# Performance work log

Measured on AMD Instinct MI355X. Metric: run time of the kernel, lower is better.

Reference implementation:

```python
import jax, jax.numpy as jnp
import numpy as np

BN_EPS = 1e-5


def _tconv(X, w1, b1, w2, b2, w3, b3):
    # X: (B, T, N, C) -> conv over time with kernel (1, k), gated GLU-style
    Xp = X.transpose(0, 2, 1, 3)  # (B, N, T, C)
    def conv(w, b):
        return jax.lax.conv_general_dilated(
            Xp, w, (1, 1), 'VALID',
            dimension_numbers=('NHWC', 'HWIO', 'NHWC')) + b
    P = conv(w1, b1)
    Q = jax.nn.sigmoid(conv(w2, b2))
    R = conv(w3, b3)
    H = jax.nn.relu(P * Q + R)
    return H.transpose(0, 2, 1, 3)  # (B, T-k+1, N, Cout)


def _cheb(x, ei, W, b):
    # Batched ChebConv (sym norm, lambda_max=2 => L_hat = -D^-1/2 A D^-1/2)
    # x: (S, N, F), ei: (S, 2, E), W: (K, F, Fout)
    S, N, F = x.shape
    row, col = ei[:, 0], ei[:, 1]           # (S, E)
    ones = jnp.ones(ei.shape[-1], x.dtype)
    def norm_one(r, c):
        deg = jax.ops.segment_sum(ones, r, num_segments=N)
        dis = jnp.where(deg > 0, jax.lax.rsqrt(jnp.maximum(deg, 1.)), 0.)
        return -dis[r] * dis[c]
    w = jax.vmap(norm_one)(row, col)        # (S, E), constant wrt floats
    def prop(xs, r, c, ws):
        return jax.ops.segment_sum(ws[:, None] * xs[c], r, num_segments=N)
    propv = jax.vmap(prop)
    Tx = [x, propv(x, row, col, w)]
    for _ in range(W.shape[0] - 2):
        Tx.append(2. * propv(Tx[-1], row, col, w) - Tx[-2])
    return jnp.einsum('ksnf,kfo->sno', jnp.stack(Tx), W) + b


def _forward(X, tc1_w1, tc1_b1, tc1_w2, tc1_b2, tc1_w3, tc1_b3,
             cheb_w, cheb_b,
             tc2_w1, tc2_b1, tc2_w2, tc2_b2, tc2_w3, tc2_b3,
             bn_gamma, bn_beta, conv3_w, conv3_b, f1_w, f1_b, edge_index):
    T0 = _tconv(X, tc1_w1, tc1_b1, tc1_w2, tc1_b2, tc1_w3, tc1_b3)  # (B,38,N,H)
    B, Tt, N, H = T0.shape
    ei = edge_index[:, :Tt].reshape(B * Tt, 2, edge_index.shape[-1])
    G = _cheb(T0.reshape(B * Tt, N, H), ei, cheb_w, cheb_b)
    G = jax.nn.relu(G.reshape(B, Tt, N, H))
    T2 = _tconv(G, tc2_w1, tc2_b1, tc2_w2, tc2_b2, tc2_w3, tc2_b3)  # (B,36,N,Co)
    # BatchNorm2d over channel dim = num_nodes (training-mode batch stats)
    Tn = T2.transpose(0, 2, 1, 3)  # (B, N, T, C)
    mean = Tn.mean(axis=(0, 2, 3), keepdims=True)
    var = Tn.var(axis=(0, 2, 3), keepdims=True)
    Tn = (Tn - mean) * jax.lax.rsqrt(var + BN_EPS)
    Tn = Tn * bn_gamma[None, :, None, None] + bn_beta[None, :, None, None]
    Tb = Tn.transpose(0, 2, 1, 3)                 # (B, T, N, C)
    Tr = Tb.reshape(B, Tb.shape[1], -1)           # (B, T, N*C=3200)
    y = jax.lax.conv_general_dilated(
        Tr[:, None, :, :], conv3_w, (1, 1), 'VALID',
        dimension_numbers=('NCHW', 'OIHW', 'NCHW'))  # (B,128,T-2,1)
    y = y + conv3_b[None, :, None, None]
    y = y[:, :, :, 0]
    pooled = y.mean(axis=2)                        # AvgPool1d over full length
    return pooled @ f1_w + f1_b                    # (B, 3200)


def setup_inputs() -> dict:
    key = jax.random.key(0)
    ks = jax.random.split(key, 20)
    B, Tw, N, Cin, H, Co, E = 32, 40, 50, 2, 128, 64, 800
    KT, K = 3, 3
    s = 0.05
    d = {
        'X': jax.random.normal(ks[0], (B, Tw, N, Cin), jnp.float32),
        'edge_index': jax.random.randint(ks[1], (B, Tw, 2, E), 0, N),
        'tc1_w1': jax.random.normal(ks[2], (1, KT, Cin, H), jnp.float32) * s,
        'tc1_b1': jnp.zeros((H,), jnp.float32),
        'tc1_w2': jax.random.normal(ks[3], (1, KT, Cin, H), jnp.float32) * s,
        'tc1_b2': jnp.zeros((H,), jnp.float32),
        'tc1_w3': jax.random.normal(ks[4], (1, KT, Cin, H), jnp.float32) * s,
        'tc1_b3': jnp.zeros((H,), jnp.float32),
        'cheb_w': jax.random.normal(ks[5], (K, H, H), jnp.float32) * s,
        'cheb_b': jnp.zeros((H,), jnp.float32),
        'tc2_w1': jax.random.normal(ks[6], (1, KT, H, Co), jnp.float32) * s,
        'tc2_b1': jnp.zeros((Co,), jnp.float32),
        'tc2_w2': jax.random.normal(ks[7], (1, KT, H, Co), jnp.float32) * s,
        'tc2_b2': jnp.zeros((Co,), jnp.float32),
        'tc2_w3': jax.random.normal(ks[8], (1, KT, H, Co), jnp.float32) * s,
        'tc2_b3': jnp.zeros((Co,), jnp.float32),
        'bn_gamma': jnp.ones((N,), jnp.float32),
        'bn_beta': jnp.zeros((N,), jnp.float32),
        'conv3_w': jax.random.normal(ks[9], (128, 1, 3, N * Co), jnp.float32) * 0.01,
        'conv3_b': jnp.zeros((128,), jnp.float32),
        'f1_w': jax.random.normal(ks[10], (128, N * Co), jnp.float32) * s,
        'f1_b': jnp.zeros((N * Co,), jnp.float32),
    }
    return d


def reference(X, tc1_w1, tc1_b1, tc1_w2, tc1_b2, tc1_w3, tc1_b3,
              cheb_w, cheb_b,
              tc2_w1, tc2_b1, tc2_w2, tc2_b2, tc2_w3, tc2_b3,
              bn_gamma, bn_beta, conv3_w, conv3_b, f1_w, f1_b, edge_index):
    return _forward(X, tc1_w1, tc1_b1, tc1_w2, tc1_b2, tc1_w3, tc1_b3,
                    cheb_w, cheb_b,
                    tc2_w1, tc2_b1, tc2_w2, tc2_b2, tc2_w3, tc2_b3,
                    bn_gamma, bn_beta, conv3_w, conv3_b, f1_w, f1_b, edge_index)
```

## Files before the change

### kernel.cpp

```cpp
#include <hip/hip_runtime.h>
#include <hip/hip_bf16.h>

#define BB 32
#define TW 40
#define NN 50
#define HH 128
#define CO 64
#define EE 800
#define TT 38
#define TT2 36
#define TPOOL 34
#define NCO 3200
#define SS (BB*TT)
#define NPAD 64
#define RPAD (SS*NPAD)

#define PB_US ((size_t)RPAD * HH)
#define PB_BYTES (PB_US * 2)

typedef __attribute__((ext_vector_type(8))) short s16x8;
typedef __attribute__((ext_vector_type(16))) float f32x16;
typedef unsigned short us;

static __device__ __forceinline__ unsigned int f2bf_u(float x) {
    unsigned int u = __float_as_uint(x);
    return (u + 0x7fffu + ((u >> 16) & 1u)) >> 16;
}
static __device__ __forceinline__ float bfu2f(unsigned int h) {
    return __uint_as_float(h << 16);
}
static __device__ __forceinline__ size_t fragoff32(int m, int c) {
    return (size_t)(c >> 4) * 512 + ((c >> 3) & 1) * 256 + m * 8 + (c & 7);
}
#define MFMA(a, b, c) __builtin_amdgcn_mfma_f32_32x32x16_bf16((a), (b), (c), 0, 0, 0)

__global__ __launch_bounds__(256) void k_wprep(
    const float* __restrict__ cw,
    const float* __restrict__ tw1, const float* __restrict__ tw2, const float* __restrict__ tw3,
    us* __restrict__ VTh, us* __restrict__ VTl,
    us* __restrict__ WTh,
    float* __restrict__ pooled)
{
    int idx = blockIdx.x * 256 + threadIdx.x;
    float v; int col, k; bool wantlo;
    us *dh, *dl;
    if (idx < 128 * 384) {
        col = idx / 384; k = idx % 384;
        if (k < 128)      v = cw[k * 128 + col] - cw[32768 + k * 128 + col];
        else if (k < 256) v = cw[16384 + (k - 128) * 128 + col];
        else              v = 2.f * cw[32768 + (k - 256) * 128 + col];
        dh = VTh; dl = VTl; wantlo = true;
    } else if (idx < 128 * 384 + 192 * 384) {
        int i2 = idx - 128 * 384;
        col = i2 / 384; k = i2 % 384;
        int gg = col >> 6, o = col & 63;
        const float* src = (gg == 0) ? tw1 : (gg == 1) ? tw2 : tw3;
        v = src[k * 64 + o];
        dh = WTh; dl = 0; wantlo = false;
    } else {
        int z = idx - (128 * 384 + 192 * 384);
        if (z < 4096) pooled[z] = 0.f;
        return;
    }
    size_t off = ((size_t)((col >> 5) * 24 + (k >> 4)) * 64 + ((k >> 3) & 1) * 32 + (col & 31)) * 8
               + (k & 7);
    unsigned int h = f2bf_u(v);
    dh[off] = (us)h;
    if (wantlo) dl[off] = (us)f2bf_u(v - bfu2f(h));
}

#define TAS 136
#define TBS 72
#define LMS 53
__global__ __launch_bounds__(256) void k_cheb(
    const int* __restrict__ EI, const float* __restrict__ X,
    const float* __restrict__ w1, const float* __restrict__ b1,
    const float* __restrict__ w2, const float* __restrict__ b2,
    const float* __restrict__ w3, const float* __restrict__ b3,
    const us* __restrict__ VTh, const us* __restrict__ VTl,
    const float* __restrict__ bias,
    us* __restrict__ Gh)
{
    __shared__ __align__(16) char smem[61440];
    us* TbA = (us*)smem;
    us* TbB = (us*)(smem + 17408);
    us* Pa  = (us*)(smem + 35840);
    float* Lm = (float*)(smem + 35840);
    us* LA  = (us*)(smem + 53248);
    float* Xs = (float*)(smem + 53248);
    int* deg  = (int*)(smem + 53248 + 1216);
    float* dis = (float*)(smem + 53248 + 1216 + 224);

    int g = blockIdx.x;
    int tid = threadIdx.x;
    int b = g / TT, t = g % TT;
    const int* row = EI + (size_t)(b * TW + t) * 2 * EE;
    const int* col = row + EE;

    {
        s16x8 zz = {0, 0, 0, 0, 0, 0, 0, 0};
        for (int i = tid; i < 2240; i += 256) ((s16x8*)smem)[i] = zz;
    }
    for (int i = tid; i < 52 * LMS; i += 256) Lm[i] = 0.f;
    for (int i = tid; i < 300; i += 256) Xs[i] = X[(size_t)(b * TW + t) * 100 + i];
    if (tid < NN) deg[tid] = 0;
    __syncthreads();

    {
        int c = tid & 127, nh = tid >> 7;
        float wr1[6], wr2[6], wr3[6];
#pragma unroll
        for (int q = 0; q < 6; q++) {
            wr1[q] = w1[q * HH + c];
            wr2[q] = w2[q * HH + c];
            wr3[q] = w3[q * HH + c];
        }
        float bv1 = b1[c], bv2 = b2[c], bv3 = b3[c];
        for (int n = nh; n < NN; n += 2) {
            float P = bv1, Q = bv2, R = bv3;
#pragma unroll
            for (int q = 0; q < 6; q++) {
                float x = Xs[(q >> 1) * 100 + n * 2 + (q & 1)];
                P += x * wr1[q]; Q += x * wr2[q]; R += x * wr3[q];
            }
            float sg = 1.f / (1.f + expf(-Q));
            float v = P * sg + R;
            v = v > 0.f ? v : 0.f;
            us h = (us)f2bf_u(v);
            TbA[n * TAS + c] = h;
            TbB[c * TBS + n] = h;
        }
    }
    __syncthreads();
    for (int e = tid; e < EE; e += 256) atomicAdd(&deg[row[e]], 1);
    __syncthreads();
    if (tid < NN) dis[tid] = deg[tid] > 0 ? rsqrtf((float)deg[tid]) : 0.f;
    __syncthreads();
    for (int e = tid; e < EE; e += 256) {
        int r = row[e], cc = col[e];
        atomicAdd(&Lm[r * LMS + cc], -dis[r] * dis[cc]);
    }
    __syncthreads();
    for (int ent = tid; ent < 512; ent += 256) {
        int lanee = ent & 63;
        int ks = (ent >> 6) & 3;
        int mt = ent >> 8;
        int m = mt * 32 + (lanee & 31);
        int kb = ks * 16 + (lanee >> 5) * 8;
        s16x8 v;
#pragma unroll
        for (int j = 0; j < 8; j++) {
            int k = kb + j;
            float lv = (m < NN && k < NN) ? Lm[m * LMS + k] : 0.f;
            v[j] = (short)f2bf_u(lv);
        }
        *(s16x8*)(LA + ent * 8) = v;
    }
    __syncthreads();

    int lane = tid & 63;
    int w = tid >> 6;
    int rg = w >> 1, fh = w & 1;
    int nl = lane & 31;
    int khalf = lane >> 5;
    size_t laneoff = (size_t)lane * 8;

    const us* vh0 = VTh + (size_t)(fh * 2) * 12288 + laneoff;
    const us* vh1 = VTh + (size_t)(fh * 2 + 1) * 12288 + laneoff;
    const us* vl0 = VTl + (size_t)(fh * 2) * 12288 + laneoff;
    const us* vl1 = VTl + (size_t)(fh * 2 + 1) * 12288 + laneoff;

    int mrowA = rg * 32 + nl;
    int kbb = khalf * 8;

    f32x16 gacc0, gacc1, d0, d1;
#pragma unroll
    for (int r = 0; r < 16; r++) { gacc0[r] = 0.f; gacc1[r] = 0.f; d0[r] = 0.f; d1[r] = 0.f; }

#pragma unroll
    for (int ks = 0; ks < 4; ks++) {
        s16x8 afr = *(const s16x8*)(LA + ((rg * 4 + ks) * 64 + lane) * 8);
        int kb = ks * 16 + kbb;
        s16x8 bf0 = *(const s16x8*)(TbB + (fh * 64 + nl) * TBS + kb);
        s16x8 bf1 = *(const s16x8*)(TbB + (fh * 64 + 32 + nl) * TBS + kb);
        d0 = MFMA(afr, bf0, d0);
        d1 = MFMA(afr, bf1, d1);
    }
#pragma unroll
    for (int ks = 0; ks < 8; ks++) {
        s16x8 ah = *(const s16x8*)(TbA + mrowA * TAS + ks * 16 + kbb);
        s16x8 bh0 = *(const s16x8*)(vh0 + ks * 512);
        s16x8 bl0 = *(const s16x8*)(vl0 + ks * 512);
        s16x8 bh1 = *(const s16x8*)(vh1 + ks * 512);
        s16x8 bl1 = *(const s16x8*)(vl1 + ks * 512);
        gacc0 = MFMA(ah, bh0, gacc0); gacc0 = MFMA(ah, bl0, gacc0);
        gacc1 = MFMA(ah, bh1, gacc1); gacc1 = MFMA(ah, bl1, gacc1);
    }
    __syncthreads();
#pragma unroll
    for (int r = 0; r < 16; r++) {
        int mrow = (r & 3) + 8 * (r >> 2) + 4 * khalf;
        int node = rg * 32 + mrow;
        int f0 = fh * 64 + nl, f1 = f0 + 32;
        us h0 = (us)f2bf_u(d0[r]);
        us h1 = (us)f2bf_u(d1[r]);
        Pa[node * TAS + f0] = h0;
        Pa[node * TAS + f1] = h1;
        TbB[f0 * TBS + node] = h0;
        TbB[f1 * TBS + node] = h1;
    }
    __syncthreads();

#pragma unroll
    for (int r = 0; r < 16; r++) { d0[r] = 0.f; d1[r] = 0.f; }
#pragma unroll
    for (int ks = 0; ks < 4; ks++) {
        s16x8 afr = *(const s16x8*)(LA + ((rg * 4 + ks) * 64 + lane) * 8);
        int kb = ks * 16 + kbb;
        s16x8 bf0 = *(const s16x8*)(TbB + (fh * 64 + nl) * TBS + kb);
        s16x8 bf1 = *(const s16x8*)(TbB + (fh * 64 + 32 + nl) * TBS + kb);
        d0 = MFMA(afr, bf0, d0);
        d1 = MFMA(afr, bf1, d1);
    }
#pragma unroll
    for (int ks = 0; ks < 8; ks++) {
        s16x8 ah = *(const s16x8*)(Pa + mrowA * TAS + ks * 16 + kbb);
        s16x8 bh0 = *(const s16x8*)(vh0 + (8 + ks) * 512);
        s16x8 bh1 = *(const s16x8*)(vh1 + (8 + ks) * 512);
        gacc0 = MFMA(ah, bh0, gacc0);
        gacc1 = MFMA(ah, bh1, gacc1);
    }
    __syncthreads();
#pragma unroll
    for (int r = 0; r < 16; r++) {
        int mrow = (r & 3) + 8 * (r >> 2) + 4 * khalf;
        int node = rg * 32 + mrow;
        int f0 = fh * 64 + nl, f1 = f0 + 32;
        Pa[node * TAS + f0] = (us)f2bf_u(d0[r]);
        Pa[node * TAS + f1] = (us)f2bf_u(d1[r]);
    }
    __syncthreads();
#pragma unroll
    for (int ks = 0; ks < 8; ks++) {
        s16x8 ah = *(const s16x8*)(Pa + mrowA * TAS + ks * 16 + kbb);
        s16x8 bh0 = *(const s16x8*)(vh0 + (16 + ks) * 512);
        s16x8 bh1 = *(const s16x8*)(vh1 + (16 + ks) * 512);
        gacc0 = MFMA(ah, bh0, gacc0);
        gacc1 = MFMA(ah, bh1, gacc1);
    }

    int c0 = fh * 64 + nl, c1 = c0 + 32;
    float bv0 = bias[c0], bv1 = bias[c1];
    size_t gb = (size_t)g * 8192 + (size_t)rg * 4096;
#pragma unroll
    for (int r = 0; r < 16; r++) {
        int mrow = (r & 3) + 8 * (r >> 2) + 4 * khalf;
        float v0 = gacc0[r] + bv0; v0 = v0 > 0.f ? v0 : 0.f;
        float v1 = gacc1[r] + bv1; v1 = v1 > 0.f ? v1 : 0.f;
        Gh[gb + fragoff32(mrow, c0)] = (us)f2bf_u(v0);
        Gh[gb + fragoff32(mrow, c1)] = (us)f2bf_u(v1);
    }
}

__global__ __launch_bounds__(128) void k_tc2(
    const us* __restrict__ Gh,
    const us* __restrict__ WTh,
    const float* __restrict__ tb1, const float* __restrict__ tb2, const float* __restrict__ tb3,
    us* __restrict__ T2)
{
    int tid = threadIdx.x;
    int lane = tid & 63;
    int w = tid >> 6;
    int nl = lane & 31;
    size_t laneoff = (size_t)lane * 8;
    int i = blockIdx.x;
    int vb = (i & 7) * 288 + (i >> 3);
    int bt36 = vb >> 1, ntile = vb & 1;
    int b = bt36 / TT2, t = bt36 % TT2;

    const us* A[3];
#pragma unroll
    for (int k3 = 0; k3 < 3; k3++)
        A[k3] = Gh + (size_t)(b * TT + t + k3) * 8192 + (size_t)ntile * 4096 + laneoff;
    const us* Bh[3];
#pragma unroll
    for (int g3 = 0; g3 < 3; g3++)
        Bh[g3] = WTh + (size_t)(g3 * 2 + w) * 12288 + laneoff;

    f32x16 aP, aQ, aR;
#pragma unroll
    for (int r = 0; r < 16; r++) { aP[r] = 0.f; aQ[r] = 0.f; aR[r] = 0.f; }

#pragma unroll
    for (int k3 = 0; k3 < 3; k3++) {
#pragma unroll
        for (int ls = 0; ls < 8; ls++) {
            int offB = (k3 * 8 + ls) * 512;
            s16x8 a0 = *(const s16x8*)(A[k3] + ls * 512);
            s16x8 ph = *(const s16x8*)(Bh[0] + offB);
            s16x8 qh = *(const s16x8*)(Bh[1] + offB);
            s16x8 rh = *(const s16x8*)(Bh[2] + offB);
            aP = MFMA(a0, ph, aP);
            aQ = MFMA(a0, qh, aQ);
            aR = MFMA(a0, rh, aR);
        }
    }

    int o = w * 32 + nl;
    float bP = tb1[o], bQ = tb2[o], bR = tb3[o];
    int rbase = (lane >> 5) * 4;
#pragma unroll
    for (int r = 0; r < 16; r++) {
        int m = (r & 3) + 8 * (r >> 2) + rbase;
        int node = ntile * 32 + m;
        if (node < NN) {
            float P = aP[r] + bP, Q = aQ[r] + bQ, R = aR[r] + bR;
            float sg = 1.f / (1.f + expf(-Q));
            float v = P * sg + R;
            v = v > 0.f ? v : 0.f;
            T2[((size_t)bt36 * NN + node) * CO + o] = (us)f2bf_u(v);
        }
    }
}

#define UPST 129
__global__ __launch_bounds__(256) void k_upool(
    const us* __restrict__ T2,
    const float* __restrict__ gamma, const float* __restrict__ beta,
    const float* __restrict__ W3, float* __restrict__ pooled)
{
    __shared__ float Ws[96 * UPST];
    __shared__ __align__(16) float Ul[96 * 36];
    __shared__ float red[512];
    int blk = blockIdx.x;
    int n = blk >> 1, jh = blk & 1;
    int tid = threadIdx.x;

    for (int i = tid; i < 12288; i += 256) {
        int ok = i >> 5, j = i & 31;
        int o = ok / 3, k = ok - 3 * o;
        Ws[(k * 32 + j) * UPST + o] = W3[(size_t)o * 9600 + k * 3200 + n * 64 + jh * 32 + j];
    }

    float s = 0.f, ss = 0.f;
    for (int i = tid; i < 9216; i += 256) {
        int bt = i >> 3, j8 = i & 7;
        s16x8 v = *(const s16x8*)(T2 + (size_t)bt * 3200 + n * 64 + j8 * 8);
#pragma unroll
        for (int j = 0; j < 8; j++) {
            float f = bfu2f((us)v[j]);
            s += f; ss += f * f;
        }
    }
    red[tid] = s; red[256 + tid] = ss;
    __syncthreads();
    for (int off = 128; off > 0; off >>= 1) {
        if (tid < off) { red[tid] += red[tid + off]; red[256 + tid] += red[256 + tid + off]; }
        __syncthreads();
    }
    const float inv = 1.f / (float)(BB * TT2 * CO);
    float mn = red[0] * inv;
    float var = red[256] * inv - mn * mn;
    float sc = rsqrtf(var + 1e-5f) * gamma[n];
    float offv = (float)TPOOL * beta[n] - (float)TPOOL * mn * sc;
    __syncthreads();

    for (int p = tid; p < 1024; p += 256) {
        int j = p & 31, b = p >> 5;
        const us* q = T2 + (size_t)b * 115200 + n * 64 + jh * 32 + j;
        float s0 = 0.f;
        for (int t = 0; t < TPOOL; t++) s0 += bfu2f(q[(size_t)t * 3200]);
        float s1 = s0 - bfu2f(q[0]) + bfu2f(q[(size_t)34 * 3200]);
        float s2 = s1 - bfu2f(q[(size_t)1 * 3200]) + bfu2f(q[(size_t)35 * 3200]);
        Ul[(0 * 32 + j) * 36 + b] = s0 * sc + offv;
        Ul[(1 * 32 + j) * 36 + b] = s1 * sc + offv;
        Ul[(2 * 32 + j) * 36 + b] = s2 * sc + offv;
    }
    __syncthreads();

    int o = tid & 127, bq = tid >> 7;
    float acc[16];
#pragma unroll
    for (int i = 0; i < 16; i++) acc[i] = 0.f;
    for (int kj = 0; kj < 96; kj++) {
        float wv = Ws[kj * UPST + o];
        const float* up = &Ul[kj * 36 + bq * 16];
#pragma unroll
        for (int i4 = 0; i4 < 4; i4++) {
            float4 u = *(const float4*)(up + i4 * 4);
            acc[i4 * 4 + 0] += wv * u.x;
            acc[i4 * 4 + 1] += wv * u.y;
            acc[i4 * 4 + 2] += wv * u.z;
            acc[i4 * 4 + 3] += wv * u.w;
        }
    }
#pragma unroll
    for (int i = 0; i < 16; i++)
        atomicAdd(&pooled[(size_t)(bq * 16 + i) * 128 + o], acc[i]);
}

__global__ __launch_bounds__(256) void k_final(
    const float* __restrict__ pooled, const float* __restrict__ b3c,
    const float* __restrict__ f1w, const float* __restrict__ f1b,
    float* __restrict__ out)
{
    int idx = blockIdx.x * 256 + threadIdx.x;
    if (idx >= BB * NCO) return;
    int q = idx % NCO;
    int b = idx / NCO;
    const float inv = 1.f / (float)TPOOL;
    float acc = f1b[q];
    const float* pp = pooled + b * 128;
#pragma unroll 4
    for (int o = 0; o < 128; o++) acc += (pp[o] * inv + b3c[o]) * f1w[(size_t)o * NCO + q];
    out[idx] = acc;
}

extern "C" void kernel_launch(void* const* d_in, const int* in_sizes, int n_in,
                              void* d_out, int out_size, void* d_ws, size_t ws_size,
                              hipStream_t stream)
{
    const float* X       = (const float*)d_in[0];
    const int*   EI      = (const int*)d_in[1];
    const float* tc1_w1  = (const float*)d_in[2];
    const float* tc1_b1  = (const float*)d_in[3];
    const float* tc1_w2  = (const float*)d_in[4];
    const float* tc1_b2  = (const float*)d_in[5];
    const float* tc1_w3  = (const float*)d_in[6];
    const float* tc1_b3  = (const float*)d_in[7];
    const float* cheb_w  = (const float*)d_in[8];
    const float* cheb_b  = (const float*)d_in[9];
    const float* tc2_w1  = (const float*)d_in[10];
    const float* tc2_b1  = (const float*)d_in[11];
    const float* tc2_w2  = (const float*)d_in[12];
    const float* tc2_b2  = (const float*)d_in[13];
    const float* tc2_w3  = (const float*)d_in[14];
    const float* tc2_b3  = (const float*)d_in[15];
    const float* bn_g    = (const float*)d_in[16];
    const float* bn_b    = (const float*)d_in[17];
    const float* conv3_w = (const float*)d_in[18];
    const float* conv3_b = (const float*)d_in[19];
    const float* f1_w    = (const float*)d_in[20];
    const float* f1_b    = (const float*)d_in[21];

    char* base = (char*)d_ws;
    us*    Gh     = (us*)base;
    us*    T2     = (us*)(base + PB_BYTES);
    float* pooled = (float*)(base + PB_BYTES + 7372800);
    us*    VTh    = (us*)(base + PB_BYTES + 7389184);
    us*    VTl    = VTh + 49152;
    us*    WTh    = VTl + 49152;

    k_wprep<<<496, 256, 0, stream>>>(cheb_w, tc2_w1, tc2_w2, tc2_w3, VTh, VTl, WTh, pooled);
    k_cheb<<<SS, 256, 0, stream>>>(EI, X, tc1_w1, tc1_b1, tc1_w2, tc1_b2, tc1_w3, tc1_b3,
                                   VTh, VTl, cheb_b, Gh);
    k_tc2<<<2304, 128, 0, stream>>>(Gh, WTh, tc2_b1, tc2_b2, tc2_b3, T2);
    k_upool<<<100, 256, 0, stream>>>(T2, bn_g, bn_b, conv3_w, pooled);
    k_final<<<(BB * NCO + 255) / 256, 256, 0, stream>>>(pooled, conv3_b, f1_w, f1_b, (float*)d_out);
}
```

Baseline: 222.1 us.

## Precompute Laplacian fragments in prep kernel, drop bf16 lo split, widen upool grid

The per-graph Laplacian build (degree, normalisation, scatter, bf16 fragment packing) moves out of the Chebyshev kernel into the prep kernel and is stored in global memory. The Chebyshev kernel then reads these fragments directly, uses less shared memory and skips several barriers. The bf16 hi/lo split of the Chebyshev weights is removed, halving the weight MFMAs and loads at some cost in accuracy. The upool kernel is split across 4x more blocks, each handling 8 batches, to raise parallelism at the cost of repeating the BN statistics and weight staging in every block.

Result: faster. 211.8 us (-4.6%).

```diff
diff --git a/kernel.cpp b/kernel.cpp
--- a/kernel.cpp
+++ b/kernel.cpp
@@ -34,76 +34,104 @@
 }
 #define MFMA(a, b, c) __builtin_amdgcn_mfma_f32_32x32x16_bf16((a), (b), (c), 0, 0, 0)
 
-__global__ __launch_bounds__(256) void k_wprep(
+__global__ __launch_bounds__(256) void k_prep(
     const float* __restrict__ cw,
     const float* __restrict__ tw1, const float* __restrict__ tw2, const float* __restrict__ tw3,
-    us* __restrict__ VTh, us* __restrict__ VTl,
-    us* __restrict__ WTh,
-    float* __restrict__ pooled)
-{
-    int idx = blockIdx.x * 256 + threadIdx.x;
-    float v; int col, k; bool wantlo;
-    us *dh, *dl;
-    if (idx < 128 * 384) {
-        col = idx / 384; k = idx % 384;
-        if (k < 128)      v = cw[k * 128 + col] - cw[32768 + k * 128 + col];
-        else if (k < 256) v = cw[16384 + (k - 128) * 128 + col];
-        else              v = 2.f * cw[32768 + (k - 256) * 128 + col];
-        dh = VTh; dl = VTl; wantlo = true;
-    } else if (idx < 128 * 384 + 192 * 384) {
-        int i2 = idx - 128 * 384;
-        col = i2 / 384; k = i2 % 384;
-        int gg = col >> 6, o = col & 63;
-        const float* src = (gg == 0) ? tw1 : (gg == 1) ? tw2 : tw3;
-        v = src[k * 64 + o];
-        dh = WTh; dl = 0; wantlo = false;
+    const int* __restrict__ EI,
+    us* __restrict__ VTh, us* __restrict__ WTh,
+    us* __restrict__ LAg, float* __restrict__ pooled)
+{
+    __shared__ float Lm[50 * 51];
+    __shared__ int   deg[NN];
+    __shared__ float dis[NN];
+    int blk = blockIdx.x;
+    int tid = threadIdx.x;
+
+    if (blk < 496) {
+        int idx = blk * 256 + tid;
+        float v; int col, k; us* dh;
+        if (idx < 128 * 384) {
+            col = idx / 384; k = idx % 384;
+            if (k < 128)      v = cw[k * 128 + col] - cw[32768 + k * 128 + col];
+            else if (k < 256) v = cw[16384 + (k - 128) * 128 + col];
+            else              v = 2.f * cw[32768 + (k - 256) * 128 + col];
+            dh = VTh;
+        } else if (idx < 128 * 384 + 192 * 384) {
+            int i2 = idx - 128 * 384;
+            col = i2 / 384; k = i2 % 384;
+            int gg = col >> 6, o = col & 63;
+            const float* src = (gg == 0) ? tw1 : (gg == 1) ? tw2 : tw3;
+            v = src[k * 64 + o];
+            dh = WTh;
+        } else {
+            int z = idx - (128 * 384 + 192 * 384);
+            if (z < 4096) pooled[z] = 0.f;
+            return;
+        }
+        size_t off = ((size_t)((col >> 5) * 24 + (k >> 4)) * 64 + ((k >> 3) & 1) * 32 + (col & 31)) * 8
+                   + (k & 7);
+        dh[off] = (us)f2bf_u(v);
     } else {
-        int z = idx - (128 * 384 + 192 * 384);
-        if (z < 4096) pooled[z] = 0.f;
-        return;
-    }
-    size_t off = ((size_t)((col >> 5) * 24 + (k >> 4)) * 64 + ((k >> 3) & 1) * 32 + (col & 31)) * 8
-               + (k & 7);
-    unsigned int h = f2bf_u(v);
-    dh[off] = (us)h;
-    if (wantlo) dl[off] = (us)f2bf_u(v - bfu2f(h));
+        int g = blk - 496;
+        int b = g / TT, t = g % TT;
+        const int* row = EI + (size_t)(b * TW + t) * 2 * EE;
+        const int* col = row + EE;
+        for (int i = tid; i < 50 * 51; i += 256) Lm[i] = 0.f;
+        if (tid < NN) deg[tid] = 0;
+        __syncthreads();
+        for (int e = tid; e < EE; e += 256) atomicAdd(&deg[row[e]], 1);
+        __syncthreads();
+        if (tid < NN) dis[tid] = deg[tid] > 0 ? rsqrtf((float)deg[tid]) : 0.f;
+        __syncthreads();
+        for (int e = tid; e < EE; e += 256) {
+            int r = row[e], cc = col[e];
+            atomicAdd(&Lm[r * 51 + cc], -dis[r] * dis[cc]);
+        }
+        __syncthreads();
+        for (int ent = tid; ent < 512; ent += 256) {
+            int lanee = ent & 63;
+            int ks = (ent >> 6) & 3;
+            int mt = ent >> 8;
+            int m = mt * 32 + (lanee & 31);
+            int kb = ks * 16 + (lanee >> 5) * 8;
+            s16x8 v;
+#pragma unroll
+            for (int j = 0; j < 8; j++) {
+                int k = kb + j;
+                float lv = (m < NN && k < NN) ? Lm[m * 51 + k] : 0.f;
+                v[j] = (short)f2bf_u(lv);
+            }
+            *(s16x8*)(LAg + (size_t)g * 4096 + ent * 8) = v;
+        }
+    }
 }
 
 #define TAS 136
 #define TBS 72
-#define LMS 53
 __global__ __launch_bounds__(256) void k_cheb(
-    const int* __restrict__ EI, const float* __restrict__ X,
+    const float* __restrict__ X,
     const float* __restrict__ w1, const float* __restrict__ b1,
     const float* __restrict__ w2, const float* __restrict__ b2,
     const float* __restrict__ w3, const float* __restrict__ b3,
-    const us* __restrict__ VTh, const us* __restrict__ VTl,
+    const us* __restrict__ VTh, const us* __restrict__ LAg,
     const float* __restrict__ bias,
     us* __restrict__ Gh)
 {
-    __shared__ __align__(16) char smem[61440];
+    __shared__ __align__(16) char smem[53248];
     us* TbA = (us*)smem;
     us* TbB = (us*)(smem + 17408);
     us* Pa  = (us*)(smem + 35840);
-    float* Lm = (float*)(smem + 35840);
-    us* LA  = (us*)(smem + 53248);
-    float* Xs = (float*)(smem + 53248);
-    int* deg  = (int*)(smem + 53248 + 1216);
-    float* dis = (float*)(smem + 53248 + 1216 + 224);
+    float* Xs = (float*)(smem + 35840);
 
     int g = blockIdx.x;
     int tid = threadIdx.x;
     int b = g / TT, t = g % TT;
-    const int* row = EI + (size_t)(b * TW + t) * 2 * EE;
-    const int* col = row + EE;
 
     {
         s16x8 zz = {0, 0, 0, 0, 0, 0, 0, 0};
         for (int i = tid; i < 2240; i += 256) ((s16x8*)smem)[i] = zz;
     }
-    for (int i = tid; i < 52 * LMS; i += 256) Lm[i] = 0.f;
     for (int i = tid; i < 300; i += 256) Xs[i] = X[(size_t)(b * TW + t) * 100 + i];
-    if (tid < NN) deg[tid] = 0;
     __syncthreads();
 
     {
@@ -132,31 +160,6 @@
         }
     }
     __syncthreads();
-    for (int e = tid; e < EE; e += 256) atomicAdd(&deg[row[e]], 1);
-    __syncthreads();
-    if (tid < NN) dis[tid] = deg[tid] > 0 ? rsqrtf((float)deg[tid]) : 0.f;
-    __syncthreads();
-    for (int e = tid; e < EE; e += 256) {
-        int r = row[e], cc = col[e];
-        atomicAdd(&Lm[r * LMS + cc], -dis[r] * dis[cc]);
-    }
-    __syncthreads();
-    for (int ent = tid; ent < 512; ent += 256) {
-        int lanee = ent & 63;
-        int ks = (ent >> 6) & 3;
-        int mt = ent >> 8;
-        int m = mt * 32 + (lanee & 31);
-        int kb = ks * 16 + (lanee >> 5) * 8;
-        s16x8 v;
-#pragma unroll
-        for (int j = 0; j < 8; j++) {
-            int k = kb + j;
-            float lv = (m < NN && k < NN) ? Lm[m * LMS + k] : 0.f;
-            v[j] = (short)f2bf_u(lv);
-        }
-        *(s16x8*)(LA + ent * 8) = v;
-    }
-    __syncthreads();
 
     int lane = tid & 63;
     int w = tid >> 6;
@@ -167,8 +170,7 @@
 
     const us* vh0 = VTh + (size_t)(fh * 2) * 12288 + laneoff;
     const us* vh1 = VTh + (size_t)(fh * 2 + 1) * 12288 + laneoff;
-    const us* vl0 = VTl + (size_t)(fh * 2) * 12288 + laneoff;
-    const us* vl1 = VTl + (size_t)(fh * 2 + 1) * 12288 + laneoff;
+    const us* lag = LAg + (size_t)g * 4096 + (size_t)rg * 2048 + laneoff;
 
     int mrowA = rg * 32 + nl;
     int kbb = khalf * 8;
@@ -179,7 +181,7 @@
 
 #pragma unroll
     for (int ks = 0; ks < 4; ks++) {
-        s16x8 afr = *(const s16x8*)(LA + ((rg * 4 + ks) * 64 + lane) * 8);
+        s16x8 afr = *(const s16x8*)(lag + ks * 512);
         int kb = ks * 16 + kbb;
         s16x8 bf0 = *(const s16x8*)(TbB + (fh * 64 + nl) * TBS + kb);
         s16x8 bf1 = *(const s16x8*)(TbB + (fh * 64 + 32 + nl) * TBS + kb);
@@ -190,11 +192,9 @@
     for (int ks = 0; ks < 8; ks++) {
         s16x8 ah = *(const s16x8*)(TbA + mrowA * TAS + ks * 16 + kbb);
         s16x8 bh0 = *(const s16x8*)(vh0 + ks * 512);
-        s16x8 bl0 = *(const s16x8*)(vl0 + ks * 512);
         s16x8 bh1 = *(const s16x8*)(vh1 + ks * 512);
-        s16x8 bl1 = *(const s16x8*)(vl1 + ks * 512);
-        gacc0 = MFMA(ah, bh0, gacc0); gacc0 = MFMA(ah, bl0, gacc0);
-        gacc1 = MFMA(ah, bh1, gacc1); gacc1 = MFMA(ah, bl1, gacc1);
+        gacc0 = MFMA(ah, bh0, gacc0);
+        gacc1 = MFMA(ah, bh1, gacc1);
     }
     __syncthreads();
 #pragma unroll
@@ -215,7 +215,7 @@
     for (int r = 0; r < 16; r++) { d0[r] = 0.f; d1[r] = 0.f; }
 #pragma unroll
     for (int ks = 0; ks < 4; ks++) {
-        s16x8 afr = *(const s16x8*)(LA + ((rg * 4 + ks) * 64 + lane) * 8);
+        s16x8 afr = *(const s16x8*)(lag + ks * 512);
         int kb = ks * 16 + kbb;
         s16x8 bf0 = *(const s16x8*)(TbB + (fh * 64 + nl) * TBS + kb);
         s16x8 bf1 = *(const s16x8*)(TbB + (fh * 64 + 32 + nl) * TBS + kb);
@@ -330,10 +330,12 @@
     const float* __restrict__ W3, float* __restrict__ pooled)
 {
     __shared__ float Ws[96 * UPST];
-    __shared__ __align__(16) float Ul[96 * 36];
+    __shared__ __align__(16) float Ul[96 * 12];
     __shared__ float red[512];
     int blk = blockIdx.x;
-    int n = blk >> 1, jh = blk & 1;
+    int n = blk >> 3;
+    int jh = (blk >> 2) & 1;
+    int bq = blk & 3;
     int tid = threadIdx.x;
 
     for (int i = tid; i < 12288; i += 256) {
@@ -365,38 +367,33 @@
     float offv = (float)TPOOL * beta[n] - (float)TPOOL * mn * sc;
     __syncthreads();
 
-    for (int p = tid; p < 1024; p += 256) {
-        int j = p & 31, b = p >> 5;
-        const us* q = T2 + (size_t)b * 115200 + n * 64 + jh * 32 + j;
+    {
+        int j = tid & 31, bl = tid >> 5;
+        int bb = bq * 8 + bl;
+        const us* q = T2 + (size_t)bb * 115200 + n * 64 + jh * 32 + j;
         float s0 = 0.f;
         for (int t = 0; t < TPOOL; t++) s0 += bfu2f(q[(size_t)t * 3200]);
         float s1 = s0 - bfu2f(q[0]) + bfu2f(q[(size_t)34 * 3200]);
         float s2 = s1 - bfu2f(q[(size_t)1 * 3200]) + bfu2f(q[(size_t)35 * 3200]);
-        Ul[(0 * 32 + j) * 36 + b] = s0 * sc + offv;
-        Ul[(1 * 32 + j) * 36 + b] = s1 * sc + offv;
-        Ul[(2 * 32 + j) * 36 + b] = s2 * sc + offv;
-    }
-    __syncthreads();
-
-    int o = tid & 127, bq = tid >> 7;
-    float acc[16];
-#pragma unroll
-    for (int i = 0; i < 16; i++) acc[i] = 0.f;
+        Ul[(0 * 32 + j) * 12 + bl] = s0 * sc + offv;
+        Ul[(1 * 32 + j) * 12 + bl] = s1 * sc + offv;
+        Ul[(2 * 32 + j) * 12 + bl] = s2 * sc + offv;
+    }
+    __syncthreads();
+
+    int o = tid & 127, bq2 = tid >> 7;
+    float acc[4] = {0.f, 0.f, 0.f, 0.f};
     for (int kj = 0; kj < 96; kj++) {
         float wv = Ws[kj * UPST + o];
-        const float* up = &Ul[kj * 36 + bq * 16];
-#pragma unroll
-        for (int i4 = 0; i4 < 4; i4++) {
-            float4 u = *(const float4*)(up + i4 * 4);
-            acc[i4 * 4 + 0] += wv * u.x;
-            acc[i4 * 4 + 1] += wv * u.y;
-            acc[i4 * 4 + 2] += wv * u.z;
-            acc[i4 * 4 + 3] += wv * u.w;
-        }
-    }
-#pragma unroll
-    for (int i = 0; i < 16; i++)
-        atomicAdd(&pooled[(size_t)(bq * 16 + i) * 128 + o], acc[i]);
+        float4 u = *(const float4*)&Ul[kj * 12 + bq2 * 4];
+        acc[0] += wv * u.x;
+        acc[1] += wv * u.y;
+        acc[2] += wv * u.z;
+        acc[3] += wv * u.w;
+    }
+#pragma unroll
+    for (int i = 0; i < 4; i++)
+        atomicAdd(&pooled[(size_t)(bq * 8 + bq2 * 4 + i) * 128 + o], acc[i]);
 }
 
 __global__ __launch_bounds__(256) void k_final(
@@ -448,13 +445,13 @@
     us*    T2     = (us*)(base + PB_BYTES);
     float* pooled = (float*)(base + PB_BYTES + 7372800);
     us*    VTh    = (us*)(base + PB_BYTES + 7389184);
-    us*    VTl    = VTh + 49152;
-    us*    WTh    = VTl + 49152;
-
-    k_wprep<<<496, 256, 0, stream>>>(cheb_w, tc2_w1, tc2_w2, tc2_w3, VTh, VTl, WTh, pooled);
-    k_cheb<<<SS, 256, 0, stream>>>(EI, X, tc1_w1, tc1_b1, tc1_w2, tc1_b2, tc1_w3, tc1_b3,
-                                   VTh, VTl, cheb_b, Gh);
+    us*    WTh    = VTh + 49152;
+    us*    LAg    = WTh + 73728;
+
+    k_prep<<<496 + SS, 256, 0, stream>>>(cheb_w, tc2_w1, tc2_w2, tc2_w3, EI, VTh, WTh, LAg, pooled);
+    k_cheb<<<SS, 256, 0, stream>>>(X, tc1_w1, tc1_b1, tc1_w2, tc1_b2, tc1_w3, tc1_b3,
+                                   VTh, LAg, cheb_b, Gh);
     k_tc2<<<2304, 128, 0, stream>>>(Gh, WTh, tc2_b1, tc2_b2, tc2_b3, T2);
-    k_upool<<<100, 256, 0, stream>>>(T2, bn_g, bn_b, conv3_w, pooled);
+    k_upool<<<400, 256, 0, stream>>>(T2, bn_g, bn_b, conv3_w, pooled);
     k_final<<<(BB * NCO + 255) / 256, 256, 0, stream>>>(pooled, conv3_b, f1_w, f1_b, (float*)d_out);
 }
```
